# Kernel tuning notes

Hardware: AMD Instinct MI355X
Metric: run time of the kernel (lower is better)

## Reference

```python
import jax, jax.numpy as jnp
import numpy as np

B, E, F, T, RANK, L = 8, 512, 1024, 2048, 10, 5


def setup_inputs() -> dict:
    key = jax.random.key(0)
    ks = jax.random.split(key, 6)
    Y = jax.random.normal(ks[0], (B, E, T), dtype=jnp.float32)
    R = jax.random.uniform(ks[1], (B, E, F), dtype=jnp.float32)
    Omega = (jax.random.uniform(ks[2], (B, E, T)) < 0.9).astype(jnp.float32)
    P0 = jax.random.normal(ks[3], (B, E, RANK), dtype=jnp.float32)
    Q0 = jax.random.normal(ks[4], (B, T, RANK), dtype=jnp.float32)
    A0 = jnp.zeros((B, F, T), dtype=jnp.float32)
    lam_log = jnp.full((L,), -5.0, dtype=jnp.float32)   # init_val=-5
    mu_log = jnp.full((L,), -5.0, dtype=jnp.float32)
    skip_logits = jnp.full((L, 3), 0.5, dtype=jnp.float32)  # skip_P, skip_Q, skip_A
    return {"Y": Y, "R": R, "Omega": Omega, "P0": P0, "Q0": Q0, "A0": A0,
            "lam_log": lam_log, "mu_log": mu_log, "skip_logits": skip_logits}


def _soft(x, t):
    return jnp.sign(x) * jnp.maximum(jnp.abs(x) - t, 0.0)


def _forward(Y, R, Omega, P0, Q0, A0, lam_log, mu_log, skip_logits):
    r = P0.shape[-1]
    I = jnp.eye(r, dtype=Y.dtype)

    def step(carry, params):
        P, Q, A = carry
        ll, ml, sk = params
        lam = jnp.exp(ll)   # lam1 == lam2 (two_lambda=False)
        mu = jnp.exp(ml)
        err = Omega * (Y - R @ A)                                   # [B,E,T]
        # --- P update: per-row masked ridge solve ---
        Mp = jnp.einsum('bet,btr,bts->bers', Omega, Q, Q) + lam * I  # [B,E,r,r]
        rhsP = jnp.einsum('bet,btr->ber', err, Q)
        P_hat = jnp.linalg.solve(Mp, rhsP[..., None])[..., 0]
        P_new = P + jax.nn.sigmoid(sk[0]) * (P_hat - P)
        # --- Q update: per-column masked ridge solve (uses P_new, same err) ---
        Mq = jnp.einsum('bet,ber,bes->btrs', Omega, P_new, P_new) + lam * I
        rhsQ = jnp.einsum('bet,ber->btr', err, P_new)
        Q_hat = jnp.linalg.solve(Mq, rhsQ[..., None])[..., 0]
        Q_new = Q + jax.nn.sigmoid(sk[1]) * (Q_hat - Q)
        # --- A update: soft-thresholded BSCA step ---
        datafit = Omega * (Y - P_new @ jnp.swapaxes(Q_new, -2, -1) - R @ A)
        A_scale = jnp.einsum('bef,bet->bft', R * R, Omega)          # [B,F,T]
        BA_temp = A_scale * A + jnp.einsum('bef,bet->bft', R, datafit)
        zero = A_scale == 0
        denom = jnp.where(zero, 1.0, A_scale)
        A_hat = jnp.where(zero, 0.0, _soft(BA_temp, mu) / denom)
        A_new = A + jax.nn.sigmoid(sk[2]) * (A_hat - A)
        return (P_new, Q_new, A_new), None

    (P, Q, A), _ = jax.lax.scan(step, (P0, Q0, A0), (lam_log, mu_log, skip_logits))
    return P, Q, A


def reference(Y, R, Omega, P0, Q0, A0, lam_log, mu_log, skip_logits):
    return _forward(Y, R, Omega, P0, Q0, A0, lam_log, mu_log, skip_logits)
```

## Files before the change

### kernel.cpp

```cpp
#include <hip/hip_runtime.h>

constexpr int B_ = 8, E_ = 512, F_ = 1024, T_ = 2048, R_ = 10, L_ = 5;
constexpr int NTRI = 55;

enum { EPI_STORE = 0, EPI_ERR = 1, EPI_AUPD = 2, EPI_AUPD0 = 3 };

__device__ __forceinline__ void solve10(float M[NTRI], const float rhs[R_],
                                        float lam, float x[R_]) {
#pragma unroll
  for (int j = 0; j < R_; j++) M[j * (j + 1) / 2 + j] += lam;
#pragma unroll
  for (int j = 0; j < R_; j++) {
    float s = M[j * (j + 1) / 2 + j];
#pragma unroll
    for (int k = 0; k < j; k++) {
      float l = M[j * (j + 1) / 2 + k];
      s -= l * l;
    }
    s = fmaxf(s, 1e-30f);
    float d = sqrtf(s);
    float inv = 1.0f / d;
    M[j * (j + 1) / 2 + j] = d;
#pragma unroll
    for (int i = j + 1; i < R_; i++) {
      float s2 = M[i * (i + 1) / 2 + j];
#pragma unroll
      for (int k = 0; k < j; k++)
        s2 -= M[i * (i + 1) / 2 + k] * M[j * (j + 1) / 2 + k];
      M[i * (i + 1) / 2 + j] = s2 * inv;
    }
  }
  float y[R_];
#pragma unroll
  for (int i = 0; i < R_; i++) {
    float s = rhs[i];
#pragma unroll
    for (int k = 0; k < i; k++) s -= M[i * (i + 1) / 2 + k] * y[k];
    y[i] = s / M[i * (i + 1) / 2 + i];
  }
#pragma unroll
  for (int ii = R_ - 1; ii >= 0; ii--) {
    float s = y[ii];
#pragma unroll
    for (int k = ii + 1; k < R_; k++) s -= M[k * (k + 1) / 2 + ii] * x[k];
    x[ii] = s / M[ii * (ii + 1) / 2 + ii];
  }
}

__device__ __forceinline__ float sigmoidf_(float v) {
  return 1.0f / (1.0f + expf(-v));
}

template <int TRANSA, int SQA, int EPI>
__global__ __launch_bounds__(256) void gemm_k(
    const float* __restrict__ Ag, const float* __restrict__ Bg,
    float* __restrict__ Cg, const float* __restrict__ aux1,
    const float* __restrict__ aux2, const float* __restrict__ mu_log,
    const float* __restrict__ sk, int step, int M, int N, int K, long sA,
    long sB, long sC) {
  int b = blockIdx.z;
  const float* A = Ag + (long)b * sA;
  const float* Bm = Bg + (long)b * sB;
  float* C = Cg + (long)b * sC;
  const float* x1 = aux1 ? aux1 + (long)b * sC : nullptr;
  const float* x2 = aux2 ? aux2 + (long)b * sC : nullptr;

  __shared__ float As[8][132];
  __shared__ float Bs[8][132];

  int tid = threadIdx.x;
  int m0 = blockIdx.y * 128, n0 = blockIdx.x * 128;
  int tx = tid & 15, ty = tid >> 4;

  float acc[8][8];
#pragma unroll
  for (int i = 0; i < 8; i++)
#pragma unroll
    for (int j = 0; j < 8; j++) acc[i][j] = 0.0f;

  int bkk = tid >> 5, bn4 = (tid & 31) << 2;
  int amm = tid >> 1, ak4 = (tid & 1) << 2;

  for (int k0 = 0; k0 < K; k0 += 8) {
    float4 bv = *reinterpret_cast<const float4*>(
        &Bm[(long)(k0 + bkk) * N + n0 + bn4]);
    *reinterpret_cast<float4*>(&Bs[bkk][bn4]) = bv;
    if (TRANSA) {
      float4 av = *reinterpret_cast<const float4*>(
          &A[(long)(k0 + bkk) * M + m0 + bn4]);
      if (SQA) {
        av.x *= av.x; av.y *= av.y; av.z *= av.z; av.w *= av.w;
      }
      *reinterpret_cast<float4*>(&As[bkk][bn4]) = av;
    } else {
      float4 av = *reinterpret_cast<const float4*>(
          &A[(long)(m0 + amm) * K + k0 + ak4]);
      As[ak4 + 0][amm] = av.x;
      As[ak4 + 1][amm] = av.y;
      As[ak4 + 2][amm] = av.z;
      As[ak4 + 3][amm] = av.w;
    }
    __syncthreads();
#pragma unroll
    for (int kk = 0; kk < 8; kk++) {
      float a[8], bb[8];
      *reinterpret_cast<float4*>(&a[0]) =
          *reinterpret_cast<const float4*>(&As[kk][ty * 8]);
      *reinterpret_cast<float4*>(&a[4]) =
          *reinterpret_cast<const float4*>(&As[kk][ty * 8 + 4]);
      *reinterpret_cast<float4*>(&bb[0]) =
          *reinterpret_cast<const float4*>(&Bs[kk][tx * 8]);
      *reinterpret_cast<float4*>(&bb[4]) =
          *reinterpret_cast<const float4*>(&Bs[kk][tx * 8 + 4]);
#pragma unroll
      for (int i = 0; i < 8; i++)
#pragma unroll
        for (int j = 0; j < 8; j++)
          acc[i][j] = fmaf(a[i], bb[j], acc[i][j]);
    }
    __syncthreads();
  }

  float mu = 0.f, s2 = 0.f;
  if (EPI == EPI_AUPD || EPI == EPI_AUPD0) {
    mu = expf(mu_log[step]);
    s2 = sigmoidf_(sk[step * 3 + 2]);
  }
#pragma unroll
  for (int i = 0; i < 8; i++) {
    int m = m0 + ty * 8 + i;
    long row = (long)m * N + n0 + tx * 8;
#pragma unroll
    for (int j4 = 0; j4 < 8; j4 += 4) {
      if (EPI == EPI_STORE) {
        float4 v;
        v.x = acc[i][j4 + 0]; v.y = acc[i][j4 + 1];
        v.z = acc[i][j4 + 2]; v.w = acc[i][j4 + 3];
        *reinterpret_cast<float4*>(&C[row + j4]) = v;
      } else if (EPI == EPI_ERR) {
        float4 om = *reinterpret_cast<const float4*>(&x1[row + j4]);
        float4 yv = *reinterpret_cast<const float4*>(&x2[row + j4]);
        float4 v;
        v.x = om.x * (yv.x - acc[i][j4 + 0]);
        v.y = om.y * (yv.y - acc[i][j4 + 1]);
        v.z = om.z * (yv.z - acc[i][j4 + 2]);
        v.w = om.w * (yv.w - acc[i][j4 + 3]);
        *reinterpret_cast<float4*>(&C[row + j4]) = v;
      } else {
        float4 as4 = *reinterpret_cast<const float4*>(&x1[row + j4]);
        float4 aold;
        if (EPI == EPI_AUPD)
          aold = *reinterpret_cast<const float4*>(&C[row + j4]);
        else {
          aold.x = 0.f; aold.y = 0.f; aold.z = 0.f; aold.w = 0.f;
        }
        float av[4], sv[4], ov[4];
        av[0] = as4.x; av[1] = as4.y; av[2] = as4.z; av[3] = as4.w;
        ov[0] = aold.x; ov[1] = aold.y; ov[2] = aold.z; ov[3] = aold.w;
#pragma unroll
        for (int c = 0; c < 4; c++) {
          float bat = fmaf(av[c], ov[c], acc[i][j4 + c]);
          float mag = fmaxf(fabsf(bat) - mu, 0.0f);
          float sft = bat > 0.f ? mag : (bat < 0.f ? -mag : 0.f);
          float ahat = (av[c] == 0.f) ? 0.f : sft / av[c];
          sv[c] = ov[c] + s2 * (ahat - ov[c]);
        }
        float4 v;
        v.x = sv[0]; v.y = sv[1]; v.z = sv[2]; v.w = sv[3];
        *reinterpret_cast<float4*>(&C[row + j4]) = v;
      }
    }
  }
}

__global__ __launch_bounds__(256) void errinit_k(float* __restrict__ err,
                                                 const float* __restrict__ Om,
                                                 const float* __restrict__ Y) {
  long i = ((long)blockIdx.x * 256 + threadIdx.x) * 4;
  float4 o = *reinterpret_cast<const float4*>(&Om[i]);
  float4 y = *reinterpret_cast<const float4*>(&Y[i]);
  float4 v;
  v.x = o.x * y.x; v.y = o.y * y.y; v.z = o.z * y.z; v.w = o.w * y.w;
  *reinterpret_cast<float4*>(&err[i]) = v;
}

__global__ __launch_bounds__(256) void p_update_k(
    const float* __restrict__ Omega, const float* __restrict__ err,
    const float* __restrict__ Qin, const float* __restrict__ Pin,
    float* __restrict__ Pout, const float* __restrict__ lam_log,
    const float* __restrict__ sk, int step) {
  int wid = (blockIdx.x << 2) + (threadIdx.x >> 6);
  int lane = threadIdx.x & 63;
  int b = wid >> 9;
  const float* om = Omega + (long)wid * T_;
  const float* er = err + (long)wid * T_;
  const float* Qb = Qin + (long)b * T_ * R_;

  float Ms[NTRI], rhs[R_], x[R_];
#pragma unroll
  for (int i = 0; i < NTRI; i++) Ms[i] = 0.f;
#pragma unroll
  for (int i = 0; i < R_; i++) rhs[i] = 0.f;

  for (int t = lane; t < T_; t += 64) {
    float w = om[t], ev = er[t];
    float q[R_];
#pragma unroll
    for (int r = 0; r < R_; r += 2) {
      float2 v = *reinterpret_cast<const float2*>(&Qb[(long)t * R_ + r]);
      q[r] = v.x; q[r + 1] = v.y;
    }
    float wq[R_];
#pragma unroll
    for (int r = 0; r < R_; r++) {
      wq[r] = w * q[r];
      rhs[r] = fmaf(ev, q[r], rhs[r]);
    }
    int idx = 0;
#pragma unroll
    for (int r = 0; r < R_; r++)
#pragma unroll
      for (int s = 0; s <= r; s++) {
        Ms[idx] = fmaf(wq[r], q[s], Ms[idx]);
        idx++;
      }
  }
#pragma unroll
  for (int off = 32; off > 0; off >>= 1) {
#pragma unroll
    for (int i = 0; i < NTRI; i++) Ms[i] += __shfl_xor(Ms[i], off, 64);
#pragma unroll
    for (int i = 0; i < R_; i++) rhs[i] += __shfl_xor(rhs[i], off, 64);
  }
  float lam = expf(lam_log[step]);
  solve10(Ms, rhs, lam, x);
  if (lane == 0) {
    float s0 = sigmoidf_(sk[step * 3 + 0]);
#pragma unroll
    for (int r = 0; r < R_; r++) {
      float pold = Pin[(long)wid * R_ + r];
      Pout[(long)wid * R_ + r] = pold + s0 * (x[r] - pold);
    }
  }
}

__global__ __launch_bounds__(256) void q_update_k(
    const float* __restrict__ Omega, const float* __restrict__ err,
    const float* __restrict__ Pn, const float* __restrict__ Qin,
    float* __restrict__ Qout, const float* __restrict__ lam_log,
    const float* __restrict__ sk, int step) {
  __shared__ float red[NTRI + R_][64];
  int b = blockIdx.x >> 5;
  int tt = blockIdx.x & 31;
  int w = threadIdx.x >> 6, lane = threadIdx.x & 63;
  int t = (tt << 6) + lane;
  const float* om = Omega + (long)b * E_ * T_ + t;
  const float* er = err + (long)b * E_ * T_ + t;
  const float* Pb = Pn + (long)b * E_ * R_;

  float Ms[NTRI], rhs[R_];
#pragma unroll
  for (int i = 0; i < NTRI; i++) Ms[i] = 0.f;
#pragma unroll
  for (int i = 0; i < R_; i++) rhs[i] = 0.f;

  for (int e = w * (E_ / 4); e < (w + 1) * (E_ / 4); e++) {
    float p[R_];
#pragma unroll
    for (int r = 0; r < R_; r += 2) {
      float2 v = *reinterpret_cast<const float2*>(&Pb[(long)e * R_ + r]);
      p[r] = v.x; p[r + 1] = v.y;
    }
    float wv = om[(long)e * T_];
    float ev = er[(long)e * T_];
    float wp[R_];
#pragma unroll
    for (int r = 0; r < R_; r++) {
      wp[r] = wv * p[r];
      rhs[r] = fmaf(ev, p[r], rhs[r]);
    }
    int idx = 0;
#pragma unroll
    for (int r = 0; r < R_; r++)
#pragma unroll
      for (int s = 0; s <= r; s++) {
        Ms[idx] = fmaf(wp[r], p[s], Ms[idx]);
        idx++;
      }
  }
  for (int ww = 0; ww < 4; ww++) {
    if (w == ww) {
      if (ww == 0) {
#pragma unroll
        for (int i = 0; i < NTRI; i++) red[i][lane] = Ms[i];
#pragma unroll
        for (int i = 0; i < R_; i++) red[NTRI + i][lane] = rhs[i];
      } else {
#pragma unroll
        for (int i = 0; i < NTRI; i++) red[i][lane] += Ms[i];
#pragma unroll
        for (int i = 0; i < R_; i++) red[NTRI + i][lane] += rhs[i];
      }
    }
    __syncthreads();
  }
  if (w == 0) {
#pragma unroll
    for (int i = 0; i < NTRI; i++) Ms[i] = red[i][lane];
#pragma unroll
    for (int i = 0; i < R_; i++) rhs[i] = red[NTRI + i][lane];
    float lam = expf(lam_log[step]);
    float x[R_];
    solve10(Ms, rhs, lam, x);
    float s1 = sigmoidf_(sk[step * 3 + 1]);
    long qi = ((long)b * T_ + t) * R_;
#pragma unroll
    for (int r = 0; r < R_; r++) {
      float qold = Qin[qi + r];
      Qout[qi + r] = qold + s1 * (x[r] - qold);
    }
  }
}

__global__ __launch_bounds__(256) void datafit_k(
    float* __restrict__ errio, const float* __restrict__ Omega,
    const float* __restrict__ Pn, const float* __restrict__ Qn) {
  int blk = blockIdx.x;
  int tch = blk & 7;
  int e = (blk >> 3) & 511;
  int b = blk >> 12;
  int t = tch * 256 + threadIdx.x;
  long base = ((long)b * E_ + e) * T_ + t;
  float p[R_];
#pragma unroll
  for (int r = 0; r < R_; r++) p[r] = Pn[((long)b * E_ + e) * R_ + r];
  float q[R_];
#pragma unroll
  for (int r = 0; r < R_; r += 2) {
    float2 v = *reinterpret_cast<const float2*>(&Qn[((long)b * T_ + t) * R_ + r]);
    q[r] = v.x; q[r + 1] = v.y;
  }
  float dot = 0.f;
#pragma unroll
  for (int r = 0; r < R_; r++) dot = fmaf(p[r], q[r], dot);
  errio[base] -= Omega[base] * dot;
}

extern "C" void kernel_launch(void* const* d_in, const int* in_sizes, int n_in,
                              void* d_out, int out_size, void* d_ws,
                              size_t ws_size, hipStream_t stream) {
  const float* Y = (const float*)d_in[0];
  const float* Rm = (const float*)d_in[1];
  const float* Om = (const float*)d_in[2];
  const float* P0 = (const float*)d_in[3];
  const float* Q0 = (const float*)d_in[4];
  const float* lam_log = (const float*)d_in[6];
  const float* mu_log = (const float*)d_in[7];
  const float* sk = (const float*)d_in[8];

  float* ws = (float*)d_ws;
  float* err = ws;
  float* Ascale = ws + (long)B_ * E_ * T_;
  float* Pa = Ascale + (long)B_ * F_ * T_;
  float* Pb = Pa + B_ * E_ * R_;
  float* Qa = Pb + B_ * E_ * R_;
  float* Qb = Qa + B_ * T_ * R_;

  float* outP = (float*)d_out;
  float* outQ = outP + B_ * E_ * R_;
  float* outA = outP + B_ * E_ * R_ + B_ * T_ * R_;

  const float* Pr[L_] = {P0, Pa, Pb, Pa, Pb};
  float* Pw[L_] = {Pa, Pb, Pa, Pb, outP};
  const float* Qr[L_] = {Q0, Qa, Qb, Qa, Qb};
  float* Qw[L_] = {Qa, Qb, Qa, Qb, outQ};

  const long sR = (long)E_ * F_;
  const long sET = (long)E_ * T_;
  const long sFT = (long)F_ * T_;

  gemm_k<1, 1, EPI_STORE><<<dim3(T_ / 128, F_ / 128, B_), 256, 0, stream>>>(
      Rm, Om, Ascale, nullptr, nullptr, nullptr, nullptr, 0, F_, T_, E_, sR,
      sET, sFT);

  for (int s = 0; s < L_; s++) {
    if (s == 0) {
      errinit_k<<<(B_ * E_ * T_) / 1024, 256, 0, stream>>>(err, Om, Y);
    } else {
      gemm_k<0, 0, EPI_ERR><<<dim3(T_ / 128, E_ / 128, B_), 256, 0, stream>>>(
          Rm, outA, err, Om, Y, nullptr, nullptr, s, E_, T_, F_, sR, sFT, sET);
    }
    p_update_k<<<(B_ * E_) / 4, 256, 0, stream>>>(Om, err, Qr[s], Pr[s], Pw[s],
                                                  lam_log, sk, s);
    q_update_k<<<B_ * (T_ / 64), 256, 0, stream>>>(Om, err, Pw[s], Qr[s],
                                                   Qw[s], lam_log, sk, s);
    datafit_k<<<B_ * E_ * (T_ / 256), 256, 0, stream>>>(err, Om, Pw[s], Qw[s]);
    if (s == 0)
      gemm_k<1, 0, EPI_AUPD0><<<dim3(T_ / 128, F_ / 128, B_), 256, 0,
                                stream>>>(Rm, err, outA, Ascale, nullptr,
                                          mu_log, sk, s, F_, T_, E_, sR, sET,
                                          sFT);
    else
      gemm_k<1, 0, EPI_AUPD><<<dim3(T_ / 128, F_ / 128, B_), 256, 0, stream>>>(
          Rm, err, outA, Ascale, nullptr, mu_log, sk, s, F_, T_, E_, sR, sET,
          sFT);
  }
}
```

Baseline: 2.792 ms.

## Rewrite GEMMs as split-bf16 MFMA kernels on transposed layouts with two-stage solves

Replaces the fp32 FMA GEMM with a 128x256x32 tiled kernel that splits each fp32 value into hi/lo bf16 parts and runs three MFMA products per fragment to keep near-fp32 accuracy. All big tensors (Omega, Y*Omega, err, A_scale, A, R) are kept in T-major transposed layouts so GEMM operands are K-contiguous. The P and Q normal-equation builds become two-stage partial-sum kernels that write to scratch, and datafit writes out-of-place. Extra transpose passes and a final per-batch transpose-and-copy of A are added, and the bf16x3 split may lose some precision relative to fp32.

```diff
diff --git a/kernel.cpp b/kernel.cpp
--- a/kernel.cpp
+++ b/kernel.cpp
@@ -2,8 +2,42 @@
 
 constexpr int B_ = 8, E_ = 512, F_ = 1024, T_ = 2048, R_ = 10, L_ = 5;
 constexpr int NTRI = 55;
+constexpr int BM_ = 128, BN_ = 256, BK_ = 32;
 
 enum { EPI_STORE = 0, EPI_ERR = 1, EPI_AUPD = 2, EPI_AUPD0 = 3 };
+
+typedef __attribute__((ext_vector_type(4))) float f32x4;
+typedef __attribute__((ext_vector_type(8))) short short8v;
+union U8 { unsigned u[4]; short8v s; };
+
+__device__ __forceinline__ unsigned bf16r(float v) {
+  unsigned u = __float_as_uint(v);
+  return (u + 0x7fffu + ((u >> 16) & 1u)) >> 16;
+}
+__device__ __forceinline__ unsigned pack1(float v) {
+  unsigned h = bf16r(v);
+  float lo = v - __uint_as_float(h << 16);
+  return h | (bf16r(lo) << 16);
+}
+__device__ __forceinline__ uint4 pack4(float4 v) {
+  uint4 r;
+  r.x = pack1(v.x); r.y = pack1(v.y); r.z = pack1(v.z); r.w = pack1(v.w);
+  return r;
+}
+__device__ __forceinline__ void unpack8(uint4 w0, uint4 w1, U8& hi, U8& lo) {
+  hi.u[0] = __builtin_amdgcn_perm(w0.y, w0.x, 0x05040100u);
+  lo.u[0] = __builtin_amdgcn_perm(w0.y, w0.x, 0x07060302u);
+  hi.u[1] = __builtin_amdgcn_perm(w0.w, w0.z, 0x05040100u);
+  lo.u[1] = __builtin_amdgcn_perm(w0.w, w0.z, 0x07060302u);
+  hi.u[2] = __builtin_amdgcn_perm(w1.y, w1.x, 0x05040100u);
+  lo.u[2] = __builtin_amdgcn_perm(w1.y, w1.x, 0x07060302u);
+  hi.u[3] = __builtin_amdgcn_perm(w1.w, w1.z, 0x05040100u);
+  lo.u[3] = __builtin_amdgcn_perm(w1.w, w1.z, 0x07060302u);
+}
+
+__device__ __forceinline__ float sigmoidf_(float v) {
+  return 1.0f / (1.0f + expf(-v));
+}
 
 __device__ __forceinline__ void solve10(float M[NTRI], const float rhs[R_],
                                         float lam, float x[R_]) {
@@ -47,78 +81,126 @@
   }
 }
 
-__device__ __forceinline__ float sigmoidf_(float v) {
-  return 1.0f / (1.0f + expf(-v));
-}
-
-template <int TRANSA, int SQA, int EPI>
-__global__ __launch_bounds__(256) void gemm_k(
+template <int MODE>
+__global__ __launch_bounds__(256) void trans_k(const float* __restrict__ in0,
+                                               const float* __restrict__ in1,
+                                               float* __restrict__ out, int Rw,
+                                               int Cl) {
+  __shared__ float tile[32][36];
+  long ib = (long)blockIdx.z * Rw * Cl;
+  int r0 = blockIdx.y * 32, c0 = blockIdx.x * 32;
+  int tid = threadIdx.x;
+  int c4 = (tid & 7) << 2, r = tid >> 3;
+  float4 v = *(const float4*)(in0 + ib + (long)(r0 + r) * Cl + c0 + c4);
+  if (MODE == 1) {
+    float4 w = *(const float4*)(in1 + ib + (long)(r0 + r) * Cl + c0 + c4);
+    v.x *= w.x; v.y *= w.y; v.z *= w.z; v.w *= w.w;
+  }
+  *(float4*)&tile[r][c4] = v;
+  __syncthreads();
+  int co = tid >> 3, ro4 = (tid & 7) << 2;
+  float4 o;
+  o.x = tile[ro4 + 0][co];
+  o.y = tile[ro4 + 1][co];
+  o.z = tile[ro4 + 2][co];
+  o.w = tile[ro4 + 3][co];
+  *(float4*)(out + ib + (long)(c0 + co) * Rw + r0 + ro4) = o;
+}
+
+template <int EPI, int SQB>
+__global__ __launch_bounds__(256, 2) void gemm_split(
     const float* __restrict__ Ag, const float* __restrict__ Bg,
     float* __restrict__ Cg, const float* __restrict__ aux1,
     const float* __restrict__ aux2, const float* __restrict__ mu_log,
     const float* __restrict__ sk, int step, int M, int N, int K, long sA,
     long sB, long sC) {
+  __shared__ unsigned As[BM_ * BK_];
+  __shared__ unsigned Bs[BN_ * BK_];
   int b = blockIdx.z;
   const float* A = Ag + (long)b * sA;
-  const float* Bm = Bg + (long)b * sB;
+  const float* Bop = Bg + (long)b * sB;
   float* C = Cg + (long)b * sC;
   const float* x1 = aux1 ? aux1 + (long)b * sC : nullptr;
   const float* x2 = aux2 ? aux2 + (long)b * sC : nullptr;
 
-  __shared__ float As[8][132];
-  __shared__ float Bs[8][132];
-
   int tid = threadIdx.x;
-  int m0 = blockIdx.y * 128, n0 = blockIdx.x * 128;
-  int tx = tid & 15, ty = tid >> 4;
-
-  float acc[8][8];
-#pragma unroll
-  for (int i = 0; i < 8; i++)
-#pragma unroll
-    for (int j = 0; j < 8; j++) acc[i][j] = 0.0f;
-
-  int bkk = tid >> 5, bn4 = (tid & 31) << 2;
-  int amm = tid >> 1, ak4 = (tid & 1) << 2;
-
-  for (int k0 = 0; k0 < K; k0 += 8) {
-    float4 bv = *reinterpret_cast<const float4*>(
-        &Bm[(long)(k0 + bkk) * N + n0 + bn4]);
-    *reinterpret_cast<float4*>(&Bs[bkk][bn4]) = bv;
-    if (TRANSA) {
-      float4 av = *reinterpret_cast<const float4*>(
-          &A[(long)(k0 + bkk) * M + m0 + bn4]);
-      if (SQA) {
-        av.x *= av.x; av.y *= av.y; av.z *= av.z; av.w *= av.w;
+  int m0 = blockIdx.y * BM_, n0 = blockIdx.x * BN_;
+  int g = tid & 7, rb = tid >> 3;
+  int g4 = g << 2;
+  int l = tid & 63, lr = l & 15, lh = l >> 4;
+  int wv = tid >> 6, wr = wv >> 1, wc = wv & 1;
+
+  f32x4 acc[4][8];
+#pragma unroll
+  for (int i = 0; i < 4; i++)
+#pragma unroll
+    for (int j = 0; j < 8; j++) acc[i][j] = {0.f, 0.f, 0.f, 0.f};
+
+  float4 va[4], vb[8];
+#pragma unroll
+  for (int p = 0; p < 4; p++)
+    va[p] = *(const float4*)&A[(long)(m0 + rb + 32 * p) * K + g4];
+#pragma unroll
+  for (int p = 0; p < 8; p++)
+    vb[p] = *(const float4*)&Bop[(long)(n0 + rb + 32 * p) * K + g4];
+
+  for (int kt = 0; kt < K; kt += BK_) {
+    uint4 pa[4], pb[8];
+#pragma unroll
+    for (int p = 0; p < 4; p++) pa[p] = pack4(va[p]);
+#pragma unroll
+    for (int p = 0; p < 8; p++) {
+      float4 v = vb[p];
+      if (SQB) { v.x *= v.x; v.y *= v.y; v.z *= v.z; v.w *= v.w; }
+      pb[p] = pack4(v);
+    }
+    __syncthreads();
+#pragma unroll
+    for (int p = 0; p < 4; p++) {
+      int row = rb + 32 * p;
+      *(uint4*)&As[row * BK_ + ((g ^ (row & 7)) << 2)] = pa[p];
+    }
+#pragma unroll
+    for (int p = 0; p < 8; p++) {
+      int row = rb + 32 * p;
+      *(uint4*)&Bs[row * BK_ + ((g ^ (row & 7)) << 2)] = pb[p];
+    }
+    __syncthreads();
+    if (kt + BK_ < K) {
+#pragma unroll
+      for (int p = 0; p < 4; p++)
+        va[p] = *(const float4*)&A[(long)(m0 + rb + 32 * p) * K + kt + BK_ + g4];
+#pragma unroll
+      for (int p = 0; p < 8; p++)
+        vb[p] = *(const float4*)&Bop[(long)(n0 + rb + 32 * p) * K + kt + BK_ + g4];
+    }
+    U8 aH[4], aL[4];
+#pragma unroll
+    for (int mf = 0; mf < 4; mf++) {
+      int m = wr * 64 + mf * 16 + lr;
+      int s7 = m & 7, g0 = 2 * lh;
+      uint4 w0 = *(const uint4*)&As[m * BK_ + ((g0 ^ s7) << 2)];
+      uint4 w1 = *(const uint4*)&As[m * BK_ + (((g0 + 1) ^ s7) << 2)];
+      unpack8(w0, w1, aH[mf], aL[mf]);
+    }
+#pragma unroll
+    for (int nf = 0; nf < 8; nf++) {
+      int n = wc * 128 + nf * 16 + lr;
+      int s7 = n & 7, g0 = 2 * lh;
+      uint4 w0 = *(const uint4*)&Bs[n * BK_ + ((g0 ^ s7) << 2)];
+      uint4 w1 = *(const uint4*)&Bs[n * BK_ + (((g0 + 1) ^ s7) << 2)];
+      U8 bH, bL;
+      unpack8(w0, w1, bH, bL);
+#pragma unroll
+      for (int mf = 0; mf < 4; mf++) {
+        acc[mf][nf] = __builtin_amdgcn_mfma_f32_16x16x32_bf16(
+            aH[mf].s, bH.s, acc[mf][nf], 0, 0, 0);
+        acc[mf][nf] = __builtin_amdgcn_mfma_f32_16x16x32_bf16(
+            aL[mf].s, bH.s, acc[mf][nf], 0, 0, 0);
+        acc[mf][nf] = __builtin_amdgcn_mfma_f32_16x16x32_bf16(
+            aH[mf].s, bL.s, acc[mf][nf], 0, 0, 0);
       }
-      *reinterpret_cast<float4*>(&As[bkk][bn4]) = av;
-    } else {
-      float4 av = *reinterpret_cast<const float4*>(
-          &A[(long)(m0 + amm) * K + k0 + ak4]);
-      As[ak4 + 0][amm] = av.x;
-      As[ak4 + 1][amm] = av.y;
-      As[ak4 + 2][amm] = av.z;
-      As[ak4 + 3][amm] = av.w;
-    }
-    __syncthreads();
-#pragma unroll
-    for (int kk = 0; kk < 8; kk++) {
-      float a[8], bb[8];
-      *reinterpret_cast<float4*>(&a[0]) =
-          *reinterpret_cast<const float4*>(&As[kk][ty * 8]);
-      *reinterpret_cast<float4*>(&a[4]) =
-          *reinterpret_cast<const float4*>(&As[kk][ty * 8 + 4]);
-      *reinterpret_cast<float4*>(&bb[0]) =
-          *reinterpret_cast<const float4*>(&Bs[kk][tx * 8]);
-      *reinterpret_cast<float4*>(&bb[4]) =
-          *reinterpret_cast<const float4*>(&Bs[kk][tx * 8 + 4]);
-#pragma unroll
-      for (int i = 0; i < 8; i++)
-#pragma unroll
-        for (int j = 0; j < 8; j++)
-          acc[i][j] = fmaf(a[i], bb[j], acc[i][j]);
-    }
-    __syncthreads();
+    }
   }
 
   float mu = 0.f, s2 = 0.f;
@@ -127,89 +209,52 @@
     s2 = sigmoidf_(sk[step * 3 + 2]);
   }
 #pragma unroll
-  for (int i = 0; i < 8; i++) {
-    int m = m0 + ty * 8 + i;
-    long row = (long)m * N + n0 + tx * 8;
-#pragma unroll
-    for (int j4 = 0; j4 < 8; j4 += 4) {
-      if (EPI == EPI_STORE) {
-        float4 v;
-        v.x = acc[i][j4 + 0]; v.y = acc[i][j4 + 1];
-        v.z = acc[i][j4 + 2]; v.w = acc[i][j4 + 3];
-        *reinterpret_cast<float4*>(&C[row + j4]) = v;
-      } else if (EPI == EPI_ERR) {
-        float4 om = *reinterpret_cast<const float4*>(&x1[row + j4]);
-        float4 yv = *reinterpret_cast<const float4*>(&x2[row + j4]);
-        float4 v;
-        v.x = om.x * (yv.x - acc[i][j4 + 0]);
-        v.y = om.y * (yv.y - acc[i][j4 + 1]);
-        v.z = om.z * (yv.z - acc[i][j4 + 2]);
-        v.w = om.w * (yv.w - acc[i][j4 + 3]);
-        *reinterpret_cast<float4*>(&C[row + j4]) = v;
-      } else {
-        float4 as4 = *reinterpret_cast<const float4*>(&x1[row + j4]);
-        float4 aold;
-        if (EPI == EPI_AUPD)
-          aold = *reinterpret_cast<const float4*>(&C[row + j4]);
-        else {
-          aold.x = 0.f; aold.y = 0.f; aold.z = 0.f; aold.w = 0.f;
+  for (int mf = 0; mf < 4; mf++) {
+#pragma unroll
+    for (int nf = 0; nf < 8; nf++) {
+#pragma unroll
+      for (int r = 0; r < 4; r++) {
+        int m = m0 + wr * 64 + mf * 16 + lh * 4 + r;
+        int n = n0 + wc * 128 + nf * 16 + lr;
+        long idx = (long)m * N + n;
+        float c = acc[mf][nf][r];
+        if (EPI == EPI_STORE) {
+          C[idx] = c;
+        } else if (EPI == EPI_ERR) {
+          C[idx] = x1[idx] - x2[idx] * c;
+        } else {
+          float asv = x1[idx];
+          float aold = (EPI == EPI_AUPD) ? C[idx] : 0.f;
+          float bat = fmaf(asv, aold, c);
+          float mag = fmaxf(fabsf(bat) - mu, 0.f);
+          float sft = copysignf(mag, bat);
+          float ahat = (asv == 0.f) ? 0.f : sft / asv;
+          C[idx] = aold + s2 * (ahat - aold);
         }
-        float av[4], sv[4], ov[4];
-        av[0] = as4.x; av[1] = as4.y; av[2] = as4.z; av[3] = as4.w;
-        ov[0] = aold.x; ov[1] = aold.y; ov[2] = aold.z; ov[3] = aold.w;
-#pragma unroll
-        for (int c = 0; c < 4; c++) {
-          float bat = fmaf(av[c], ov[c], acc[i][j4 + c]);
-          float mag = fmaxf(fabsf(bat) - mu, 0.0f);
-          float sft = bat > 0.f ? mag : (bat < 0.f ? -mag : 0.f);
-          float ahat = (av[c] == 0.f) ? 0.f : sft / av[c];
-          sv[c] = ov[c] + s2 * (ahat - ov[c]);
-        }
-        float4 v;
-        v.x = sv[0]; v.y = sv[1]; v.z = sv[2]; v.w = sv[3];
-        *reinterpret_cast<float4*>(&C[row + j4]) = v;
       }
     }
   }
 }
 
-__global__ __launch_bounds__(256) void errinit_k(float* __restrict__ err,
-                                                 const float* __restrict__ Om,
-                                                 const float* __restrict__ Y) {
-  long i = ((long)blockIdx.x * 256 + threadIdx.x) * 4;
-  float4 o = *reinterpret_cast<const float4*>(&Om[i]);
-  float4 y = *reinterpret_cast<const float4*>(&Y[i]);
-  float4 v;
-  v.x = o.x * y.x; v.y = o.y * y.y; v.z = o.z * y.z; v.w = o.w * y.w;
-  *reinterpret_cast<float4*>(&err[i]) = v;
-}
-
-__global__ __launch_bounds__(256) void p_update_k(
-    const float* __restrict__ Omega, const float* __restrict__ err,
-    const float* __restrict__ Qin, const float* __restrict__ Pin,
-    float* __restrict__ Pout, const float* __restrict__ lam_log,
-    const float* __restrict__ sk, int step) {
-  int wid = (blockIdx.x << 2) + (threadIdx.x >> 6);
-  int lane = threadIdx.x & 63;
-  int b = wid >> 9;
-  const float* om = Omega + (long)wid * T_;
-  const float* er = err + (long)wid * T_;
-  const float* Qb = Qin + (long)b * T_ * R_;
-
-  float Ms[NTRI], rhs[R_], x[R_];
+__global__ __launch_bounds__(256) void p_stage1(const float* __restrict__ errT,
+                                                const float* __restrict__ OmT,
+                                                const float* __restrict__ Q,
+                                                float* __restrict__ scr) {
+  int tc = blockIdx.x, eb = blockIdx.y, b = blockIdx.z;
+  int e = eb * 256 + threadIdx.x;
+  float Ms[NTRI], rhs[R_];
 #pragma unroll
   for (int i = 0; i < NTRI; i++) Ms[i] = 0.f;
 #pragma unroll
   for (int i = 0; i < R_; i++) rhs[i] = 0.f;
-
-  for (int t = lane; t < T_; t += 64) {
-    float w = om[t], ev = er[t];
+  long base = (long)b * T_ * E_ + e;
+  for (int t = tc * 128; t < tc * 128 + 128; ++t) {
+    const float* qr = Q + ((long)b * T_ + t) * R_;
     float q[R_];
 #pragma unroll
-    for (int r = 0; r < R_; r += 2) {
-      float2 v = *reinterpret_cast<const float2*>(&Qb[(long)t * R_ + r]);
-      q[r] = v.x; q[r + 1] = v.y;
-    }
+    for (int r = 0; r < R_; r++) q[r] = qr[r];
+    float w = OmT[base + (long)t * E_];
+    float ev = errT[base + (long)t * E_];
     float wq[R_];
 #pragma unroll
     for (int r = 0; r < R_; r++) {
@@ -225,58 +270,64 @@
         idx++;
       }
   }
-#pragma unroll
-  for (int off = 32; off > 0; off >>= 1) {
-#pragma unroll
-    for (int i = 0; i < NTRI; i++) Ms[i] += __shfl_xor(Ms[i], off, 64);
-#pragma unroll
-    for (int i = 0; i < R_; i++) rhs[i] += __shfl_xor(rhs[i], off, 64);
+  long so = ((long)b * 16 + tc) * 65 * E_ + e;
+#pragma unroll
+  for (int i = 0; i < NTRI; i++) scr[so + (long)i * E_] = Ms[i];
+#pragma unroll
+  for (int i = 0; i < R_; i++) scr[so + (long)(NTRI + i) * E_] = rhs[i];
+}
+
+__global__ __launch_bounds__(256) void p_stage2(
+    const float* __restrict__ scr, const float* __restrict__ Pin,
+    float* __restrict__ Pout, const float* __restrict__ lam_log,
+    const float* __restrict__ sk, int step) {
+  int idx = blockIdx.x * 256 + threadIdx.x;
+  int b = idx >> 9, e = idx & 511;
+  float Ms[NTRI], rhs[R_], x[R_];
+#pragma unroll
+  for (int i = 0; i < NTRI; i++) Ms[i] = 0.f;
+#pragma unroll
+  for (int i = 0; i < R_; i++) rhs[i] = 0.f;
+  for (int tc = 0; tc < 16; ++tc) {
+    long so = ((long)b * 16 + tc) * 65 * E_ + e;
+#pragma unroll
+    for (int i = 0; i < NTRI; i++) Ms[i] += scr[so + (long)i * E_];
+#pragma unroll
+    for (int i = 0; i < R_; i++) rhs[i] += scr[so + (long)(NTRI + i) * E_];
   }
   float lam = expf(lam_log[step]);
   solve10(Ms, rhs, lam, x);
-  if (lane == 0) {
-    float s0 = sigmoidf_(sk[step * 3 + 0]);
+  float s0 = sigmoidf_(sk[step * 3 + 0]);
+#pragma unroll
+  for (int r = 0; r < R_; r++) {
+    float pold = Pin[(long)idx * R_ + r];
+    Pout[(long)idx * R_ + r] = pold + s0 * (x[r] - pold);
+  }
+}
+
+__global__ __launch_bounds__(256) void q_stage1(const float* __restrict__ errT,
+                                                const float* __restrict__ OmT,
+                                                const float* __restrict__ Pn,
+                                                float* __restrict__ scr) {
+  int ec = blockIdx.x, tb = blockIdx.y, b = blockIdx.z;
+  int t = tb * 256 + threadIdx.x;
+  float Ms[NTRI], rhs[R_];
+#pragma unroll
+  for (int i = 0; i < NTRI; i++) Ms[i] = 0.f;
+#pragma unroll
+  for (int i = 0; i < R_; i++) rhs[i] = 0.f;
+  long base = ((long)b * T_ + t) * E_;
+  for (int e = ec * 128; e < ec * 128 + 128; ++e) {
+    const float* pr = Pn + ((long)b * E_ + e) * R_;
+    float p[R_];
+#pragma unroll
+    for (int r = 0; r < R_; r++) p[r] = pr[r];
+    float w = OmT[base + e];
+    float ev = errT[base + e];
+    float wp[R_];
 #pragma unroll
     for (int r = 0; r < R_; r++) {
-      float pold = Pin[(long)wid * R_ + r];
-      Pout[(long)wid * R_ + r] = pold + s0 * (x[r] - pold);
-    }
-  }
-}
-
-__global__ __launch_bounds__(256) void q_update_k(
-    const float* __restrict__ Omega, const float* __restrict__ err,
-    const float* __restrict__ Pn, const float* __restrict__ Qin,
-    float* __restrict__ Qout, const float* __restrict__ lam_log,
-    const float* __restrict__ sk, int step) {
-  __shared__ float red[NTRI + R_][64];
-  int b = blockIdx.x >> 5;
-  int tt = blockIdx.x & 31;
-  int w = threadIdx.x >> 6, lane = threadIdx.x & 63;
-  int t = (tt << 6) + lane;
-  const float* om = Omega + (long)b * E_ * T_ + t;
-  const float* er = err + (long)b * E_ * T_ + t;
-  const float* Pb = Pn + (long)b * E_ * R_;
-
-  float Ms[NTRI], rhs[R_];
-#pragma unroll
-  for (int i = 0; i < NTRI; i++) Ms[i] = 0.f;
-#pragma unroll
-  for (int i = 0; i < R_; i++) rhs[i] = 0.f;
-
-  for (int e = w * (E_ / 4); e < (w + 1) * (E_ / 4); e++) {
-    float p[R_];
-#pragma unroll
-    for (int r = 0; r < R_; r += 2) {
-      float2 v = *reinterpret_cast<const float2*>(&Pb[(long)e * R_ + r]);
-      p[r] = v.x; p[r + 1] = v.y;
-    }
-    float wv = om[(long)e * T_];
-    float ev = er[(long)e * T_];
-    float wp[R_];
-#pragma unroll
-    for (int r = 0; r < R_; r++) {
-      wp[r] = wv * p[r];
+      wp[r] = w * p[r];
       rhs[r] = fmaf(ev, p[r], rhs[r]);
     }
     int idx = 0;
@@ -288,62 +339,58 @@
         idx++;
       }
   }
-  for (int ww = 0; ww < 4; ww++) {
-    if (w == ww) {
-      if (ww == 0) {
-#pragma unroll
-        for (int i = 0; i < NTRI; i++) red[i][lane] = Ms[i];
-#pragma unroll
-        for (int i = 0; i < R_; i++) red[NTRI + i][lane] = rhs[i];
-      } else {
-#pragma unroll
-        for (int i = 0; i < NTRI; i++) red[i][lane] += Ms[i];
-#pragma unroll
-        for (int i = 0; i < R_; i++) red[NTRI + i][lane] += rhs[i];
-      }
-    }
-    __syncthreads();
-  }
-  if (w == 0) {
-#pragma unroll
-    for (int i = 0; i < NTRI; i++) Ms[i] = red[i][lane];
-#pragma unroll
-    for (int i = 0; i < R_; i++) rhs[i] = red[NTRI + i][lane];
-    float lam = expf(lam_log[step]);
-    float x[R_];
-    solve10(Ms, rhs, lam, x);
-    float s1 = sigmoidf_(sk[step * 3 + 1]);
-    long qi = ((long)b * T_ + t) * R_;
-#pragma unroll
-    for (int r = 0; r < R_; r++) {
-      float qold = Qin[qi + r];
-      Qout[qi + r] = qold + s1 * (x[r] - qold);
-    }
+  long so = ((long)b * 4 + ec) * 65 * T_ + t;
+#pragma unroll
+  for (int i = 0; i < NTRI; i++) scr[so + (long)i * T_] = Ms[i];
+#pragma unroll
+  for (int i = 0; i < R_; i++) scr[so + (long)(NTRI + i) * T_] = rhs[i];
+}
+
+__global__ __launch_bounds__(256) void q_stage2(
+    const float* __restrict__ scr, const float* __restrict__ Qin,
+    float* __restrict__ Qout, const float* __restrict__ lam_log,
+    const float* __restrict__ sk, int step) {
+  int idx = blockIdx.x * 256 + threadIdx.x;
+  int b = idx >> 11, t = idx & 2047;
+  float Ms[NTRI], rhs[R_], x[R_];
+#pragma unroll
+  for (int i = 0; i < NTRI; i++) Ms[i] = 0.f;
+#pragma unroll
+  for (int i = 0; i < R_; i++) rhs[i] = 0.f;
+  for (int ec = 0; ec < 4; ++ec) {
+    long so = ((long)b * 4 + ec) * 65 * T_ + t;
+#pragma unroll
+    for (int i = 0; i < NTRI; i++) Ms[i] += scr[so + (long)i * T_];
+#pragma unroll
+    for (int i = 0; i < R_; i++) rhs[i] += scr[so + (long)(NTRI + i) * T_];
+  }
+  float lam = expf(lam_log[step]);
+  solve10(Ms, rhs, lam, x);
+  float s1 = sigmoidf_(sk[step * 3 + 1]);
+#pragma unroll
+  for (int r = 0; r < R_; r++) {
+    float qold = Qin[(long)idx * R_ + r];
+    Qout[(long)idx * R_ + r] = qold + s1 * (x[r] - qold);
   }
 }
 
 __global__ __launch_bounds__(256) void datafit_k(
-    float* __restrict__ errio, const float* __restrict__ Omega,
-    const float* __restrict__ Pn, const float* __restrict__ Qn) {
-  int blk = blockIdx.x;
-  int tch = blk & 7;
-  int e = (blk >> 3) & 511;
-  int b = blk >> 12;
-  int t = tch * 256 + threadIdx.x;
-  long base = ((long)b * E_ + e) * T_ + t;
+    const float* __restrict__ errIn, float* __restrict__ errOut,
+    const float* __restrict__ OmT, const float* __restrict__ Pn,
+    const float* __restrict__ Qn) {
+  int tc = blockIdx.x, eb = blockIdx.y, b = blockIdx.z;
+  int e = eb * 256 + threadIdx.x;
   float p[R_];
 #pragma unroll
   for (int r = 0; r < R_; r++) p[r] = Pn[((long)b * E_ + e) * R_ + r];
-  float q[R_];
-#pragma unroll
-  for (int r = 0; r < R_; r += 2) {
-    float2 v = *reinterpret_cast<const float2*>(&Qn[((long)b * T_ + t) * R_ + r]);
-    q[r] = v.x; q[r + 1] = v.y;
-  }
-  float dot = 0.f;
-#pragma unroll
-  for (int r = 0; r < R_; r++) dot = fmaf(p[r], q[r], dot);
-  errio[base] -= Omega[base] * dot;
+  for (int t = tc * 16; t < tc * 16 + 16; ++t) {
+    const float* qr = Qn + ((long)b * T_ + t) * R_;
+    float dot = 0.f;
+#pragma unroll
+    for (int r = 0; r < R_; r++) dot = fmaf(p[r], qr[r], dot);
+    long ix = ((long)b * T_ + t) * E_ + e;
+    errOut[ix] = errIn[ix] - OmT[ix] * dot;
+  }
 }
 
 extern "C" void kernel_launch(void* const* d_in, const int* in_sizes, int n_in,
@@ -359,50 +406,64 @@
   const float* sk = (const float*)d_in[8];
 
   float* ws = (float*)d_ws;
-  float* err = ws;
-  float* Ascale = ws + (long)B_ * E_ * T_;
-  float* Pa = Ascale + (long)B_ * F_ * T_;
+  float* OmT = ws;
+  float* YOm = OmT + (long)B_ * T_ * E_;
+  float* errT = YOm + (long)B_ * T_ * E_;
+  float* AscT = errT + (long)B_ * T_ * E_;
+  float* Rt = AscT + (long)B_ * T_ * F_;
+  float* Pa = Rt + (long)B_ * F_ * E_;
   float* Pb = Pa + B_ * E_ * R_;
   float* Qa = Pb + B_ * E_ * R_;
   float* Qb = Qa + B_ * T_ * R_;
+  float* scr = Qb + B_ * T_ * R_;
 
   float* outP = (float*)d_out;
   float* outQ = outP + B_ * E_ * R_;
-  float* outA = outP + B_ * E_ * R_ + B_ * T_ * R_;
+  float* AT = outQ + B_ * T_ * R_;
 
   const float* Pr[L_] = {P0, Pa, Pb, Pa, Pb};
   float* Pw[L_] = {Pa, Pb, Pa, Pb, outP};
   const float* Qr[L_] = {Q0, Qa, Qb, Qa, Qb};
   float* Qw[L_] = {Qa, Qb, Qa, Qb, outQ};
 
-  const long sR = (long)E_ * F_;
-  const long sET = (long)E_ * T_;
-  const long sFT = (long)F_ * T_;
-
-  gemm_k<1, 1, EPI_STORE><<<dim3(T_ / 128, F_ / 128, B_), 256, 0, stream>>>(
-      Rm, Om, Ascale, nullptr, nullptr, nullptr, nullptr, 0, F_, T_, E_, sR,
-      sET, sFT);
-
-  for (int s = 0; s < L_; s++) {
-    if (s == 0) {
-      errinit_k<<<(B_ * E_ * T_) / 1024, 256, 0, stream>>>(err, Om, Y);
-    } else {
-      gemm_k<0, 0, EPI_ERR><<<dim3(T_ / 128, E_ / 128, B_), 256, 0, stream>>>(
-          Rm, outA, err, Om, Y, nullptr, nullptr, s, E_, T_, F_, sR, sFT, sET);
-    }
-    p_update_k<<<(B_ * E_) / 4, 256, 0, stream>>>(Om, err, Qr[s], Pr[s], Pw[s],
-                                                  lam_log, sk, s);
-    q_update_k<<<B_ * (T_ / 64), 256, 0, stream>>>(Om, err, Pw[s], Qr[s],
-                                                   Qw[s], lam_log, sk, s);
-    datafit_k<<<B_ * E_ * (T_ / 256), 256, 0, stream>>>(err, Om, Pw[s], Qw[s]);
+  dim3 blk(256);
+  trans_k<0><<<dim3(T_ / 32, E_ / 32, B_), blk, 0, stream>>>(Om, nullptr, OmT,
+                                                             E_, T_);
+  trans_k<1><<<dim3(T_ / 32, E_ / 32, B_), blk, 0, stream>>>(Y, Om, YOm, E_,
+                                                             T_);
+  trans_k<0><<<dim3(F_ / 32, E_ / 32, B_), blk, 0, stream>>>(Rm, nullptr, Rt,
+                                                             E_, F_);
+  gemm_split<EPI_STORE, 1><<<dim3(F_ / BN_, T_ / BM_, B_), blk, 0, stream>>>(
+      OmT, Rt, AscT, nullptr, nullptr, nullptr, nullptr, 0, T_, F_, E_,
+      (long)T_ * E_, (long)F_ * E_, (long)T_ * F_);
+
+  for (int s = 0; s < L_; ++s) {
+    const float* errS = (s == 0) ? YOm : errT;
+    if (s > 0) {
+      gemm_split<EPI_ERR, 0><<<dim3(E_ / BN_, T_ / BM_, B_), blk, 0, stream>>>(
+          AT, Rm, errT, YOm, OmT, nullptr, nullptr, s, T_, E_, F_,
+          (long)T_ * F_, (long)E_ * F_, (long)T_ * E_);
+    }
+    p_stage1<<<dim3(16, 2, B_), blk, 0, stream>>>(errS, OmT, Qr[s], scr);
+    p_stage2<<<16, blk, 0, stream>>>(scr, Pr[s], Pw[s], lam_log, sk, s);
+    q_stage1<<<dim3(4, 8, B_), blk, 0, stream>>>(errS, OmT, Pw[s], scr);
+    q_stage2<<<64, blk, 0, stream>>>(scr, Qr[s], Qw[s], lam_log, sk, s);
+    datafit_k<<<dim3(128, 2, B_), blk, 0, stream>>>(errS, errT, OmT, Pw[s],
+                                                    Qw[s]);
     if (s == 0)
-      gemm_k<1, 0, EPI_AUPD0><<<dim3(T_ / 128, F_ / 128, B_), 256, 0,
-                                stream>>>(Rm, err, outA, Ascale, nullptr,
-                                          mu_log, sk, s, F_, T_, E_, sR, sET,
-                                          sFT);
+      gemm_split<EPI_AUPD0, 0>
+          <<<dim3(F_ / BN_, T_ / BM_, B_), blk, 0, stream>>>(
+              errT, Rt, AT, AscT, nullptr, mu_log, sk, s, T_, F_, E_,
+              (long)T_ * E_, (long)F_ * E_, (long)T_ * F_);
     else
-      gemm_k<1, 0, EPI_AUPD><<<dim3(T_ / 128, F_ / 128, B_), 256, 0, stream>>>(
-          Rm, err, outA, Ascale, nullptr, mu_log, sk, s, F_, T_, E_, sR, sET,
-          sFT);
-  }
-}
+      gemm_split<EPI_AUPD, 0><<<dim3(F_ / BN_, T_ / BM_, B_), blk, 0, stream>>>(
+          errT, Rt, AT, AscT, nullptr, mu_log, sk, s, T_, F_, E_,
+          (long)T_ * E_, (long)F_ * E_, (long)T_ * F_);
+  }
+  for (int b = 0; b < B_; ++b) {
+    trans_k<0><<<dim3(F_ / 32, T_ / 32, 1), blk, 0, stream>>>(
+        AT + (long)b * T_ * F_, nullptr, scr, T_, F_);
+    hipMemcpyAsync(AT + (long)b * T_ * F_, scr, (long)T_ * F_ * sizeof(float),
+                   hipMemcpyDeviceToDevice, stream);
+  }
+}
```

New measurement: 2.423 ms. 1.15x faster.
